# Performance work log

Measured on AMD Instinct MI355X. Metric: run time of the kernel, lower is better.

Reference implementation:

```python
import jax, jax.numpy as jnp
import numpy as np

B, D, N, K = 4, 256, 4096, 8192


def setup_inputs() -> dict:
    key = jax.random.key(0)
    kx, ke = jax.random.split(key)
    x = jax.random.normal(kx, (B, D, N), dtype=jnp.float32)
    e = jax.random.normal(ke, (K, D), dtype=jnp.float32)
    return {"x": x, "e": e}


def reference(x, e):
    # encode: cdist(x^T [B,N,D], e [K,D]) -> [B,N,K]; argmin over K.
    # sqrt is monotonic, so argmin of squared distance == argmin of cdist.
    xt = jnp.transpose(x, (0, 2, 1))                      # [B,N,D]
    x2 = jnp.sum(xt * xt, axis=-1, keepdims=True)         # [B,N,1]
    e2 = jnp.sum(e * e, axis=-1)                          # [K]
    d2 = x2 - 2.0 * jnp.einsum('bnd,kd->bnk', xt, e) + e2 # [B,N,K]
    codes = jnp.argmin(d2, axis=-1)                       # [B,N]
    # decode: embedding gather then transpose back to [B,D,N]
    quantized = e[codes]                                  # [B,N,D]
    return jnp.transpose(quantized, (0, 2, 1))            # [B,D,N]
```

## Files before the change

### kernel.cpp

```cpp
#include <hip/hip_runtime.h>
#include <stdint.h>

#define B_ 4
#define D_ 256
#define N_ 4096
#define K_ 8192
#define Q_ (B_*N_)

#define KSPLIT_ 4
#define KSLICE_ (K_/KSPLIT_)
#define CHUNK_ 64
#define NCHUNK_ (KSLICE_/CHUNK_)
#define QTILE_ 256

typedef __attribute__((ext_vector_type(8))) short bf16x8;
typedef __attribute__((ext_vector_type(16))) float f32x16;
typedef __attribute__((ext_vector_type(4))) unsigned short us4;

__device__ __forceinline__ unsigned short f32_to_bf16(float f) {
  unsigned u = __float_as_uint(f);
  unsigned r = 0x7FFFu + ((u >> 16) & 1u);
  return (unsigned short)((u + r) >> 16);
}
__device__ __forceinline__ float bf16_to_f32(unsigned short h) {
  return __uint_as_float(((unsigned)h) << 16);
}

__device__ __forceinline__ void gl_lds16(const void* g, void* l) {
  __builtin_amdgcn_global_load_lds(
      (const __attribute__((address_space(1))) unsigned int*)g,
      (__attribute__((address_space(3))) unsigned int*)l, 16, 0, 0);
}

__global__ __launch_bounds__(512) void prep_kernel(
    const float* __restrict__ x, const float* __restrict__ e,
    unsigned short* __restrict__ xh, unsigned short* __restrict__ xl,
    unsigned short* __restrict__ eh, unsigned short* __restrict__ el,
    float* __restrict__ e2h, unsigned long long* __restrict__ keys) {
  __shared__ float tile[64][260];
  const int t = threadIdx.x;
  const int w = t >> 6;
  const int lam = t & 63;

  if (blockIdx.x < 256) {
    const int b = blockIdx.x >> 6;
    const int n0 = (blockIdx.x & 63) << 6;
#pragma unroll
    for (int p = 0; p < 4; ++p) {
      const int d = p * 64 + (t >> 3);
      const int f4 = t & 7;
      const float* src = x + (size_t)(b * D_ + d) * N_ + n0;
      float4 v1 = *(const float4*)(src + f4 * 4);
      float4 v2 = *(const float4*)(src + 32 + f4 * 4);
      tile[f4 * 4 + 0][d] = v1.x; tile[f4 * 4 + 1][d] = v1.y;
      tile[f4 * 4 + 2][d] = v1.z; tile[f4 * 4 + 3][d] = v1.w;
      tile[32 + f4 * 4 + 0][d] = v2.x; tile[32 + f4 * 4 + 1][d] = v2.y;
      tile[32 + f4 * 4 + 2][d] = v2.z; tile[32 + f4 * 4 + 3][d] = v2.w;
    }
    __syncthreads();
#pragma unroll
    for (int i = 0; i < 8; ++i) {
      const int q = w * 8 + i;
      float4 v = *(const float4*)&tile[q][lam * 4];
      unsigned short h0 = f32_to_bf16(v.x), h1 = f32_to_bf16(v.y);
      unsigned short h2 = f32_to_bf16(v.z), h3 = f32_to_bf16(v.w);
      us4 hv = {h0, h1, h2, h3};
      us4 lv = {f32_to_bf16(v.x - bf16_to_f32(h0)),
                f32_to_bf16(v.y - bf16_to_f32(h1)),
                f32_to_bf16(v.z - bf16_to_f32(h2)),
                f32_to_bf16(v.w - bf16_to_f32(h3))};
      const size_t qg = (size_t)b * N_ + n0 + q;
      *(us4*)(xh + qg * D_ + lam * 4) = hv;
      *(us4*)(xl + qg * D_ + lam * 4) = lv;
    }
  } else {
    const int k0 = ((int)blockIdx.x - 256) * 8;
    const int k = k0 + w;
    float4 v = *(const float4*)(e + (size_t)k * D_ + lam * 4);
    unsigned short h0 = f32_to_bf16(v.x), h1 = f32_to_bf16(v.y);
    unsigned short h2 = f32_to_bf16(v.z), h3 = f32_to_bf16(v.w);
    us4 hv = {h0, h1, h2, h3};
    us4 lv = {f32_to_bf16(v.x - bf16_to_f32(h0)),
              f32_to_bf16(v.y - bf16_to_f32(h1)),
              f32_to_bf16(v.z - bf16_to_f32(h2)),
              f32_to_bf16(v.w - bf16_to_f32(h3))};
    *(us4*)(eh + (size_t)k * D_ + lam * 4) = hv;
    *(us4*)(el + (size_t)k * D_ + lam * 4) = lv;
    float sq = v.x * v.x + v.y * v.y + v.z * v.z + v.w * v.w;
#pragma unroll
    for (int xm = 1; xm <= 32; xm <<= 1) sq += __shfl_xor(sq, xm, 64);
    if (lam == 0) e2h[k] = 0.5f * sq;
    if (t < 16) keys[(size_t)k0 * 2 + t] = ~0ull;
  }
}

__global__ __launch_bounds__(512, 2) void vq_main_kernel(
    const unsigned short* __restrict__ xh, const unsigned short* __restrict__ xl,
    const unsigned short* __restrict__ eh, const unsigned short* __restrict__ el,
    const float* __restrict__ e2h, unsigned long long* __restrict__ keys) {
  __shared__ __attribute__((aligned(16))) unsigned short Bs[2][2][CHUNK_ * 256];

  const int tid = threadIdx.x;
  const int w = tid >> 6;
  const int lane = tid & 63;
  const int l = lane & 31;
  const int hi = lane >> 5;

  const int qt = blockIdx.x >> 2;
  const int ksl = blockIdx.x & 3;
  const int q0 = qt * QTILE_;
  const int kbase = ksl * KSLICE_;
  const int qw = q0 + w * 32;

  bf16x8 ah[16], al[16];
  {
    const unsigned short* pa = xh + (size_t)(qw + l) * D_ + hi * 8;
    const unsigned short* pb = xl + (size_t)(qw + l) * D_ + hi * 8;
#pragma unroll
    for (int kc16 = 0; kc16 < 16; ++kc16) {
      ah[kc16] = *(const bf16x8*)(pa + kc16 * 16);
      al[kc16] = *(const bf16x8*)(pb + kc16 * 16);
    }
  }

  float rminv[16];
  unsigned rmp[4];
#pragma unroll
  for (int r = 0; r < 16; ++r) rminv[r] = __builtin_inff();
#pragma unroll
  for (int i = 0; i < 4; ++i) rmp[i] = 0u;

  auto stage = [&](int ch, int buf) {
    const int kc = kbase + ch * CHUNK_;
#pragma unroll
    for (int p = 0; p < 4; ++p) {
      const int c0 = w * 8 + p * 2;
      const int c = c0 + hi;
      const int g = l ^ (c & 31);
      const size_t srcoff = (size_t)(kc + c) * D_ + g * 8;
      gl_lds16(eh + srcoff, &Bs[buf][0][c0 * 256]);
      gl_lds16(el + srcoff, &Bs[buf][1][c0 * 256]);
    }
  };

  stage(0, 0);

#pragma unroll 1
  for (int ch = 0; ch < NCHUNK_; ++ch) {
    const int buf = ch & 1;
    __syncthreads();
    if (ch + 1 < NCHUNK_) stage(ch + 1, buf ^ 1);
    const int kc = kbase + ch * CHUNK_;
    const float e2v0 = e2h[kc + l];
    const float e2v1 = e2h[kc + 32 + l];

    const unsigned short* bh_base = &Bs[buf][0][0];
    const unsigned short* bl_base = &Bs[buf][1][0];
#define RD(base, kk) \
    (*(const bf16x8*)&(base)[(((kk) >> 4) * 32 + l) * 256 + \
                             (((((kk) & 15) * 2 + hi) ^ l) * 8)])

    f32x16 acc0, acc1;
#pragma unroll
    for (int r = 0; r < 16; ++r) { acc0[r] = 0.f; acc1[r] = 0.f; }

    bf16x8 cbh = RD(bh_base, 0), cbl = RD(bl_base, 0);
    bf16x8 nbh = RD(bh_base, 1), nbl = RD(bl_base, 1);
#pragma unroll
    for (int kk = 0; kk < 32; ++kk) {
      const bf16x8 ubh = cbh, ubl = cbl;
      cbh = nbh; cbl = nbl;
      if (kk + 2 < 32) { nbh = RD(bh_base, kk + 2); nbl = RD(bl_base, kk + 2); }
      const int ks = kk & 15;
      if (kk < 16) {
        acc0 = __builtin_amdgcn_mfma_f32_32x32x16_bf16(ah[ks], ubh, acc0, 0, 0, 0);
        acc0 = __builtin_amdgcn_mfma_f32_32x32x16_bf16(ah[ks], ubl, acc0, 0, 0, 0);
        acc0 = __builtin_amdgcn_mfma_f32_32x32x16_bf16(al[ks], ubh, acc0, 0, 0, 0);
      } else {
        acc1 = __builtin_amdgcn_mfma_f32_32x32x16_bf16(ah[ks], ubh, acc1, 0, 0, 0);
        acc1 = __builtin_amdgcn_mfma_f32_32x32x16_bf16(ah[ks], ubl, acc1, 0, 0, 0);
        acc1 = __builtin_amdgcn_mfma_f32_32x32x16_bf16(al[ks], ubh, acc1, 0, 0, 0);
      }
      if (kk == 15) {
        const unsigned vc = (unsigned)(ch * 2 + 0);
#pragma unroll
        for (int r = 0; r < 16; ++r) {
          float dv = e2v0 - acc0[r];
          bool better = dv < rminv[r];
          rminv[r] = better ? dv : rminv[r];
          const unsigned sh = (r & 3) * 8;
          unsigned np = (rmp[r >> 2] & ~(0xFFu << sh)) | (vc << sh);
          rmp[r >> 2] = better ? np : rmp[r >> 2];
        }
      }
    }
#undef RD
    {
      const unsigned vc = (unsigned)(ch * 2 + 1);
#pragma unroll
      for (int r = 0; r < 16; ++r) {
        float dv = e2v1 - acc1[r];
        bool better = dv < rminv[r];
        rminv[r] = better ? dv : rminv[r];
        const unsigned sh = (r & 3) * 8;
        unsigned np = (rmp[r >> 2] & ~(0xFFu << sh)) | (vc << sh);
        rmp[r >> 2] = better ? np : rmp[r >> 2];
      }
    }
  }

#pragma unroll
  for (int r = 0; r < 16; ++r) {
    float bv = rminv[r];
    const unsigned sh = (r & 3) * 8;
    int bi = kbase + (int)((rmp[r >> 2] >> sh) & 0xFFu) * 32 + l;
#pragma unroll
    for (int xm = 1; xm <= 16; xm <<= 1) {
      float ov = __shfl_xor(bv, xm, 64);
      int oi = __shfl_xor(bi, xm, 64);
      if (ov < bv || (ov == bv && oi < bi)) { bv = ov; bi = oi; }
    }
    if (l == 0) {
      const int m = (r & 3) + 8 * (r >> 2) + 4 * hi;
      const int qq = qw + m;
      unsigned su = __float_as_uint(bv);
      su ^= (unsigned)(((int)su >> 31) | 0x80000000u);
      unsigned long long key = ((unsigned long long)su << 32) | (unsigned)bi;
      atomicMin(keys + qq, key);
    }
  }
}

__global__ __launch_bounds__(256) void decode_kernel(
    const unsigned long long* __restrict__ keys,
    const float* __restrict__ e, float* __restrict__ out) {
  __shared__ float tile[32][260];
  __shared__ int codes[32];
  const int t = threadIdx.x;
  const int b = blockIdx.y;
  const int n0 = blockIdx.x * 32;
  const int w = t >> 6, lam = t & 63;
  if (t < 32)
    codes[t] = (int)(keys[(size_t)b * N_ + n0 + t] & 0xFFFFFFFFull);
  __syncthreads();
#pragma unroll
  for (int i = 0; i < 8; ++i) {
    const int row = w * 8 + i;
    float4 ev = *(const float4*)(e + (size_t)codes[row] * D_ + lam * 4);
    *(float4*)&tile[row][lam * 4] = ev;
  }
  __syncthreads();
#pragma unroll
  for (int iter = 0; iter < 8; ++iter) {
    const int d = iter * 32 + (t >> 3);
    const int nc = (t & 7) * 4;
    float4 ov = {tile[nc][d], tile[nc + 1][d], tile[nc + 2][d], tile[nc + 3][d]};
    *(float4*)(out + (size_t)(b * D_ + d) * N_ + n0 + nc) = ov;
  }
}

extern "C" void kernel_launch(void* const* d_in, const int* in_sizes, int n_in,
                              void* d_out, int out_size, void* d_ws, size_t ws_size,
                              hipStream_t stream) {
  const float* x = (const float*)d_in[0];
  const float* e = (const float*)d_in[1];
  float* out = (float*)d_out;

  char* wksp = (char*)d_ws;
  unsigned short* xh = (unsigned short*)wksp;
  unsigned short* xl = xh + (size_t)Q_ * D_;
  unsigned short* eh = xl + (size_t)Q_ * D_;
  unsigned short* el = eh + (size_t)K_ * D_;
  float* e2h = (float*)(el + (size_t)K_ * D_);
  unsigned long long* keys = (unsigned long long*)(e2h + K_);

  prep_kernel<<<1280, 512, 0, stream>>>(x, e, xh, xl, eh, el, e2h, keys);
  vq_main_kernel<<<(Q_ / QTILE_) * KSPLIT_, 512, 0, stream>>>(xh, xl, eh, el, e2h, keys);
  decode_kernel<<<dim3(N_ / 32, B_), 256, 0, stream>>>(keys, e, out);
}
```

Before: 247.7 us.

## Drop LDS staging; each wave handles 64 queries, reading codebook from global

Removes the double-buffered LDS staging of codebook chunks and the per-chunk __syncthreads. Each wave now streams codebook rows directly from global memory into registers. Each wave covers two 32-query tiles, so every B fragment feeds twice as many MFMAs, and the block drops to 256 threads with 1 block per CU. This cuts LDS traffic and barrier stalls, but risks global-load latency exposure, higher register pressure (64 A-fragment vectors) and lower occupancy.

```diff
diff --git a/kernel.cpp b/kernel.cpp
--- a/kernel.cpp
+++ b/kernel.cpp
@@ -9,8 +9,7 @@
 
 #define KSPLIT_ 4
 #define KSLICE_ (K_/KSPLIT_)
-#define CHUNK_ 64
-#define NCHUNK_ (KSLICE_/CHUNK_)
+#define NCHUNK_ 64
 #define QTILE_ 256
 
 typedef __attribute__((ext_vector_type(8))) short bf16x8;
@@ -24,12 +23,6 @@
 }
 __device__ __forceinline__ float bf16_to_f32(unsigned short h) {
   return __uint_as_float(((unsigned)h) << 16);
-}
-
-__device__ __forceinline__ void gl_lds16(const void* g, void* l) {
-  __builtin_amdgcn_global_load_lds(
-      (const __attribute__((address_space(1))) unsigned int*)g,
-      (__attribute__((address_space(3))) unsigned int*)l, 16, 0, 0);
 }
 
 __global__ __launch_bounds__(512) void prep_kernel(
@@ -94,12 +87,10 @@
   }
 }
 
-__global__ __launch_bounds__(512, 2) void vq_main_kernel(
+__global__ __launch_bounds__(256, 1) void vq_main_kernel(
     const unsigned short* __restrict__ xh, const unsigned short* __restrict__ xl,
     const unsigned short* __restrict__ eh, const unsigned short* __restrict__ el,
     const float* __restrict__ e2h, unsigned long long* __restrict__ keys) {
-  __shared__ __attribute__((aligned(16))) unsigned short Bs[2][2][CHUNK_ * 256];
-
   const int tid = threadIdx.x;
   const int w = tid >> 6;
   const int lane = tid & 63;
@@ -108,125 +99,116 @@
 
   const int qt = blockIdx.x >> 2;
   const int ksl = blockIdx.x & 3;
-  const int q0 = qt * QTILE_;
   const int kbase = ksl * KSLICE_;
-  const int qw = q0 + w * 32;
-
-  bf16x8 ah[16], al[16];
+  const int qw = qt * QTILE_ + w * 64;
+
+  bf16x8 ah0[16], al0[16], ah1[16], al1[16];
   {
-    const unsigned short* pa = xh + (size_t)(qw + l) * D_ + hi * 8;
-    const unsigned short* pb = xl + (size_t)(qw + l) * D_ + hi * 8;
+    const unsigned short* p0h = xh + (size_t)(qw + l) * D_ + hi * 8;
+    const unsigned short* p0l = xl + (size_t)(qw + l) * D_ + hi * 8;
+    const unsigned short* p1h = xh + (size_t)(qw + 32 + l) * D_ + hi * 8;
+    const unsigned short* p1l = xl + (size_t)(qw + 32 + l) * D_ + hi * 8;
 #pragma unroll
     for (int kc16 = 0; kc16 < 16; ++kc16) {
-      ah[kc16] = *(const bf16x8*)(pa + kc16 * 16);
-      al[kc16] = *(const bf16x8*)(pb + kc16 * 16);
-    }
-  }
-
-  float rminv[16];
-  unsigned rmp[4];
-#pragma unroll
-  for (int r = 0; r < 16; ++r) rminv[r] = __builtin_inff();
-#pragma unroll
-  for (int i = 0; i < 4; ++i) rmp[i] = 0u;
-
-  auto stage = [&](int ch, int buf) {
-    const int kc = kbase + ch * CHUNK_;
-#pragma unroll
-    for (int p = 0; p < 4; ++p) {
-      const int c0 = w * 8 + p * 2;
-      const int c = c0 + hi;
-      const int g = l ^ (c & 31);
-      const size_t srcoff = (size_t)(kc + c) * D_ + g * 8;
-      gl_lds16(eh + srcoff, &Bs[buf][0][c0 * 256]);
-      gl_lds16(el + srcoff, &Bs[buf][1][c0 * 256]);
-    }
-  };
-
-  stage(0, 0);
+      ah0[kc16] = *(const bf16x8*)(p0h + kc16 * 16);
+      al0[kc16] = *(const bf16x8*)(p0l + kc16 * 16);
+      ah1[kc16] = *(const bf16x8*)(p1h + kc16 * 16);
+      al1[kc16] = *(const bf16x8*)(p1l + kc16 * 16);
+    }
+  }
+
+  float rminv0[16], rminv1[16];
+  unsigned rmp0[4], rmp1[4];
+#pragma unroll
+  for (int r = 0; r < 16; ++r) { rminv0[r] = __builtin_inff(); rminv1[r] = __builtin_inff(); }
+#pragma unroll
+  for (int i = 0; i < 4; ++i) { rmp0[i] = 0u; rmp1[i] = 0u; }
+
+  const unsigned short* pbh = eh + (size_t)(kbase + l) * D_ + hi * 8;
+  const unsigned short* pbl = el + (size_t)(kbase + l) * D_ + hi * 8;
 
 #pragma unroll 1
   for (int ch = 0; ch < NCHUNK_; ++ch) {
-    const int buf = ch & 1;
-    __syncthreads();
-    if (ch + 1 < NCHUNK_) stage(ch + 1, buf ^ 1);
-    const int kc = kbase + ch * CHUNK_;
-    const float e2v0 = e2h[kc + l];
-    const float e2v1 = e2h[kc + 32 + l];
-
-    const unsigned short* bh_base = &Bs[buf][0][0];
-    const unsigned short* bl_base = &Bs[buf][1][0];
-#define RD(base, kk) \
-    (*(const bf16x8*)&(base)[(((kk) >> 4) * 32 + l) * 256 + \
-                             (((((kk) & 15) * 2 + hi) ^ l) * 8)])
+    const unsigned short* ph = pbh + (size_t)ch * 32 * D_;
+    const unsigned short* pl = pbl + (size_t)ch * 32 * D_;
+    const float e2v = e2h[kbase + ch * 32 + l];
 
     f32x16 acc0, acc1;
 #pragma unroll
     for (int r = 0; r < 16; ++r) { acc0[r] = 0.f; acc1[r] = 0.f; }
 
-    bf16x8 cbh = RD(bh_base, 0), cbl = RD(bl_base, 0);
-    bf16x8 nbh = RD(bh_base, 1), nbl = RD(bl_base, 1);
-#pragma unroll
-    for (int kk = 0; kk < 32; ++kk) {
+    bf16x8 cbh = *(const bf16x8*)(ph);
+    bf16x8 cbl = *(const bf16x8*)(pl);
+    bf16x8 nbh = *(const bf16x8*)(ph + 16);
+    bf16x8 nbl = *(const bf16x8*)(pl + 16);
+#pragma unroll
+    for (int ks = 0; ks < 16; ++ks) {
       const bf16x8 ubh = cbh, ubl = cbl;
       cbh = nbh; cbl = nbl;
-      if (kk + 2 < 32) { nbh = RD(bh_base, kk + 2); nbl = RD(bl_base, kk + 2); }
-      const int ks = kk & 15;
-      if (kk < 16) {
-        acc0 = __builtin_amdgcn_mfma_f32_32x32x16_bf16(ah[ks], ubh, acc0, 0, 0, 0);
-        acc0 = __builtin_amdgcn_mfma_f32_32x32x16_bf16(ah[ks], ubl, acc0, 0, 0, 0);
-        acc0 = __builtin_amdgcn_mfma_f32_32x32x16_bf16(al[ks], ubh, acc0, 0, 0, 0);
-      } else {
-        acc1 = __builtin_amdgcn_mfma_f32_32x32x16_bf16(ah[ks], ubh, acc1, 0, 0, 0);
-        acc1 = __builtin_amdgcn_mfma_f32_32x32x16_bf16(ah[ks], ubl, acc1, 0, 0, 0);
-        acc1 = __builtin_amdgcn_mfma_f32_32x32x16_bf16(al[ks], ubh, acc1, 0, 0, 0);
-      }
-      if (kk == 15) {
-        const unsigned vc = (unsigned)(ch * 2 + 0);
-#pragma unroll
-        for (int r = 0; r < 16; ++r) {
-          float dv = e2v0 - acc0[r];
-          bool better = dv < rminv[r];
-          rminv[r] = better ? dv : rminv[r];
-          const unsigned sh = (r & 3) * 8;
-          unsigned np = (rmp[r >> 2] & ~(0xFFu << sh)) | (vc << sh);
-          rmp[r >> 2] = better ? np : rmp[r >> 2];
-        }
-      }
-    }
-#undef RD
+      if (ks + 2 < 16) {
+        nbh = *(const bf16x8*)(ph + (ks + 2) * 16);
+        nbl = *(const bf16x8*)(pl + (ks + 2) * 16);
+      }
+      acc0 = __builtin_amdgcn_mfma_f32_32x32x16_bf16(ah0[ks], ubh, acc0, 0, 0, 0);
+      acc1 = __builtin_amdgcn_mfma_f32_32x32x16_bf16(ah1[ks], ubh, acc1, 0, 0, 0);
+      acc0 = __builtin_amdgcn_mfma_f32_32x32x16_bf16(ah0[ks], ubl, acc0, 0, 0, 0);
+      acc1 = __builtin_amdgcn_mfma_f32_32x32x16_bf16(ah1[ks], ubl, acc1, 0, 0, 0);
+      acc0 = __builtin_amdgcn_mfma_f32_32x32x16_bf16(al0[ks], ubh, acc0, 0, 0, 0);
+      acc1 = __builtin_amdgcn_mfma_f32_32x32x16_bf16(al1[ks], ubh, acc1, 0, 0, 0);
+    }
+
+    const unsigned vc = (unsigned)ch;
+#pragma unroll
+    for (int r = 0; r < 16; ++r) {
+      const unsigned sh = (r & 3) * 8;
+      float dv0 = e2v - acc0[r];
+      bool b0 = dv0 < rminv0[r];
+      rminv0[r] = b0 ? dv0 : rminv0[r];
+      unsigned np0 = (rmp0[r >> 2] & ~(0xFFu << sh)) | (vc << sh);
+      rmp0[r >> 2] = b0 ? np0 : rmp0[r >> 2];
+      float dv1 = e2v - acc1[r];
+      bool b1 = dv1 < rminv1[r];
+      rminv1[r] = b1 ? dv1 : rminv1[r];
+      unsigned np1 = (rmp1[r >> 2] & ~(0xFFu << sh)) | (vc << sh);
+      rmp1[r >> 2] = b1 ? np1 : rmp1[r >> 2];
+    }
+  }
+
+#pragma unroll
+  for (int r = 0; r < 16; ++r) {
+    const int m = (r & 3) + 8 * (r >> 2) + 4 * hi;
+    const unsigned sh = (r & 3) * 8;
     {
-      const unsigned vc = (unsigned)(ch * 2 + 1);
-#pragma unroll
-      for (int r = 0; r < 16; ++r) {
-        float dv = e2v1 - acc1[r];
-        bool better = dv < rminv[r];
-        rminv[r] = better ? dv : rminv[r];
-        const unsigned sh = (r & 3) * 8;
-        unsigned np = (rmp[r >> 2] & ~(0xFFu << sh)) | (vc << sh);
-        rmp[r >> 2] = better ? np : rmp[r >> 2];
-      }
-    }
-  }
-
-#pragma unroll
-  for (int r = 0; r < 16; ++r) {
-    float bv = rminv[r];
-    const unsigned sh = (r & 3) * 8;
-    int bi = kbase + (int)((rmp[r >> 2] >> sh) & 0xFFu) * 32 + l;
-#pragma unroll
-    for (int xm = 1; xm <= 16; xm <<= 1) {
-      float ov = __shfl_xor(bv, xm, 64);
-      int oi = __shfl_xor(bi, xm, 64);
-      if (ov < bv || (ov == bv && oi < bi)) { bv = ov; bi = oi; }
-    }
-    if (l == 0) {
-      const int m = (r & 3) + 8 * (r >> 2) + 4 * hi;
-      const int qq = qw + m;
-      unsigned su = __float_as_uint(bv);
-      su ^= (unsigned)(((int)su >> 31) | 0x80000000u);
-      unsigned long long key = ((unsigned long long)su << 32) | (unsigned)bi;
-      atomicMin(keys + qq, key);
+      float bv = rminv0[r];
+      int bi = kbase + (int)((rmp0[r >> 2] >> sh) & 0xFFu) * 32 + l;
+#pragma unroll
+      for (int xm = 1; xm <= 16; xm <<= 1) {
+        float ov = __shfl_xor(bv, xm, 64);
+        int oi = __shfl_xor(bi, xm, 64);
+        if (ov < bv || (ov == bv && oi < bi)) { bv = ov; bi = oi; }
+      }
+      if (l == 0) {
+        unsigned su = __float_as_uint(bv);
+        su ^= (unsigned)(((int)su >> 31) | 0x80000000u);
+        unsigned long long key = ((unsigned long long)su << 32) | (unsigned)bi;
+        atomicMin(keys + (qw + m), key);
+      }
+    }
+    {
+      float bv = rminv1[r];
+      int bi = kbase + (int)((rmp1[r >> 2] >> sh) & 0xFFu) * 32 + l;
+#pragma unroll
+      for (int xm = 1; xm <= 16; xm <<= 1) {
+        float ov = __shfl_xor(bv, xm, 64);
+        int oi = __shfl_xor(bi, xm, 64);
+        if (ov < bv || (ov == bv && oi < bi)) { bv = ov; bi = oi; }
+      }
+      if (l == 0) {
+        unsigned su = __float_as_uint(bv);
+        su ^= (unsigned)(((int)su >> 31) | 0x80000000u);
+        unsigned long long key = ((unsigned long long)su << 32) | (unsigned)bi;
+        atomicMin(keys + (qw + 32 + m), key);
+      }
     }
   }
 }
@@ -275,6 +257,6 @@
   unsigned long long* keys = (unsigned long long*)(e2h + K_);
 
   prep_kernel<<<1280, 512, 0, stream>>>(x, e, xh, xl, eh, el, e2h, keys);
-  vq_main_kernel<<<(Q_ / QTILE_) * KSPLIT_, 512, 0, stream>>>(xh, xl, eh, el, e2h, keys);
+  vq_main_kernel<<<(Q_ / QTILE_) * KSPLIT_, 256, 0, stream>>>(xh, xl, eh, el, e2h, keys);
   decode_kernel<<<dim3(N_ / 32, B_), 256, 0, stream>>>(keys, e, out);
 }
```

Result: slower. 370.2 us (+49.5%).

## Load codebook low-part directly from global in MFMA-fragment layout, halving LDS staging

Applied to the files above, without the earlier changes.

The prep kernel now writes the bf16 low part of the codebook in a pre-swizzled layout that matches the per-lane MFMA B-operand fragment order. The main kernel reads that low part straight from global memory (L2-resident) with a three-deep register prefetch, and stages only the high part through LDS. This halves LDS footprint and LDS read/write traffic per chunk, which could allow more occupancy or fewer LDS stalls. The cost is global-load latency inside the inner MFMA loop, which is only partly hidden by the prefetch, plus extra register pressure.

```diff
diff --git a/kernel.cpp b/kernel.cpp
--- a/kernel.cpp
+++ b/kernel.cpp
@@ -35,7 +35,7 @@
 __global__ __launch_bounds__(512) void prep_kernel(
     const float* __restrict__ x, const float* __restrict__ e,
     unsigned short* __restrict__ xh, unsigned short* __restrict__ xl,
-    unsigned short* __restrict__ eh, unsigned short* __restrict__ el,
+    unsigned short* __restrict__ eh, unsigned short* __restrict__ el2,
     float* __restrict__ e2h, unsigned long long* __restrict__ keys) {
   __shared__ float tile[64][260];
   const int t = threadIdx.x;
@@ -85,7 +85,11 @@
               f32_to_bf16(v.z - bf16_to_f32(h2)),
               f32_to_bf16(v.w - bf16_to_f32(h3))};
     *(us4*)(eh + (size_t)k * D_ + lam * 4) = hv;
-    *(us4*)(el + (size_t)k * D_ + lam * 4) = lv;
+    const int d = lam * 4;
+    const size_t paddr =
+        ((size_t)((k >> 5) * 16 + (d >> 4)) * 32 + (k & 31)) * 16 +
+        ((d >> 3) & 1) * 8 + (d & 7);
+    *(us4*)(el2 + paddr) = lv;
     float sq = v.x * v.x + v.y * v.y + v.z * v.z + v.w * v.w;
 #pragma unroll
     for (int xm = 1; xm <= 32; xm <<= 1) sq += __shfl_xor(sq, xm, 64);
@@ -96,9 +100,9 @@
 
 __global__ __launch_bounds__(512, 2) void vq_main_kernel(
     const unsigned short* __restrict__ xh, const unsigned short* __restrict__ xl,
-    const unsigned short* __restrict__ eh, const unsigned short* __restrict__ el,
+    const unsigned short* __restrict__ eh, const unsigned short* __restrict__ el2,
     const float* __restrict__ e2h, unsigned long long* __restrict__ keys) {
-  __shared__ __attribute__((aligned(16))) unsigned short Bs[2][2][CHUNK_ * 256];
+  __shared__ __attribute__((aligned(16))) unsigned short Bs[2][CHUNK_ * 256];
 
   const int tid = threadIdx.x;
   const int w = tid >> 6;
@@ -138,10 +142,15 @@
       const int c = c0 + hi;
       const int g = l ^ (c & 31);
       const size_t srcoff = (size_t)(kc + c) * D_ + g * 8;
-      gl_lds16(eh + srcoff, &Bs[buf][0][c0 * 256]);
-      gl_lds16(el + srcoff, &Bs[buf][1][c0 * 256]);
+      gl_lds16(eh + srcoff, &Bs[buf][c0 * 256]);
     }
   };
+
+  const unsigned short* pbl = el2 + (size_t)kbase * 256 + l * 16 + hi * 8;
+#define BL(kk) (*(const bf16x8*)(pbl + \
+    (size_t)(((ch * 2 + ((kk) >> 4)) * 16 + ((kk) & 15)) * 512)))
+#define RD(kk) (*(const bf16x8*)&Bs[buf][(((kk) >> 4) * 32 + l) * 256 + \
+    (((((kk) & 15) * 2 + hi) ^ l) * 8)])
 
   stage(0, 0);
 
@@ -154,23 +163,17 @@
     const float e2v0 = e2h[kc + l];
     const float e2v1 = e2h[kc + 32 + l];
 
-    const unsigned short* bh_base = &Bs[buf][0][0];
-    const unsigned short* bl_base = &Bs[buf][1][0];
-#define RD(base, kk) \
-    (*(const bf16x8*)&(base)[(((kk) >> 4) * 32 + l) * 256 + \
-                             (((((kk) & 15) * 2 + hi) ^ l) * 8)])
-
     f32x16 acc0, acc1;
 #pragma unroll
     for (int r = 0; r < 16; ++r) { acc0[r] = 0.f; acc1[r] = 0.f; }
 
-    bf16x8 cbh = RD(bh_base, 0), cbl = RD(bl_base, 0);
-    bf16x8 nbh = RD(bh_base, 1), nbl = RD(bl_base, 1);
+    bf16x8 cbh = RD(0), nbh = RD(1);
+    bf16x8 cbl = BL(0), nbl = BL(1), mbl = BL(2);
 #pragma unroll
     for (int kk = 0; kk < 32; ++kk) {
       const bf16x8 ubh = cbh, ubl = cbl;
-      cbh = nbh; cbl = nbl;
-      if (kk + 2 < 32) { nbh = RD(bh_base, kk + 2); nbl = RD(bl_base, kk + 2); }
+      cbh = nbh; if (kk + 2 < 32) nbh = RD(kk + 2);
+      cbl = nbl; nbl = mbl; if (kk + 3 < 32) mbl = BL(kk + 3);
       const int ks = kk & 15;
       if (kk < 16) {
         acc0 = __builtin_amdgcn_mfma_f32_32x32x16_bf16(ah[ks], ubh, acc0, 0, 0, 0);
@@ -195,6 +198,7 @@
       }
     }
 #undef RD
+#undef BL
     {
       const unsigned vc = (unsigned)(ch * 2 + 1);
 #pragma unroll
@@ -270,11 +274,11 @@
   unsigned short* xh = (unsigned short*)wksp;
   unsigned short* xl = xh + (size_t)Q_ * D_;
   unsigned short* eh = xl + (size_t)Q_ * D_;
-  unsigned short* el = eh + (size_t)K_ * D_;
-  float* e2h = (float*)(el + (size_t)K_ * D_);
+  unsigned short* el2 = eh + (size_t)K_ * D_;
+  float* e2h = (float*)(el2 + (size_t)K_ * D_);
   unsigned long long* keys = (unsigned long long*)(e2h + K_);
 
-  prep_kernel<<<1280, 512, 0, stream>>>(x, e, xh, xl, eh, el, e2h, keys);
-  vq_main_kernel<<<(Q_ / QTILE_) * KSPLIT_, 512, 0, stream>>>(xh, xl, eh, el, e2h, keys);
+  prep_kernel<<<1280, 512, 0, stream>>>(x, e, xh, xl, eh, el2, e2h, keys);
+  vq_main_kernel<<<(Q_ / QTILE_) * KSPLIT_, 512, 0, stream>>>(xh, xl, eh, el2, e2h, keys);
   decode_kernel<<<dim3(N_ / 32, B_), 256, 0, stream>>>(keys, e, out);
 }
```

After: 264.3 us. +6.7%, slower.
